# Optimization experiments

Measured on AMD Instinct MI355X. Metric: run time of the kernel, lower is better.

## Reference

```python
import jax, jax.numpy as jnp
import numpy as np

EPS = 1e-5

def _bn(x, g, b, m, v):
    inv = g / jnp.sqrt(v + EPS)
    return x * inv[None, :, None, None] + (b - m * inv)[None, :, None, None]

def _box_conv(x, y_min, y_max, x_min, x_max):
    # Learnable box filter via integral image + bilinear-interpolated corners.
    # x: (N, C, H, W); box params: (C, B). Output: (N, C*B, H, W), area-normalized.
    N, C, H, W = x.shape
    B = y_min.shape[1]
    # padded integral image (N, C, H+1, W+1)
    I = jnp.pad(jnp.cumsum(jnp.cumsum(x, axis=2), axis=3), ((0, 0), (0, 0), (1, 0), (1, 0)))
    iy = jnp.arange(H, dtype=x.dtype)
    ix = jnp.arange(W, dtype=x.dtype)

    def one_box(Ic, ymn, ymx, xmn, xmx):
        # Ic: (N, H+1, W+1); scalar box extents
        y1 = jnp.clip(iy + ymn, 0.0, H)
        y2 = jnp.clip(iy + ymx + 1.0, 0.0, H)
        x1 = jnp.clip(ix + xmn, 0.0, W)
        x2 = jnp.clip(ix + xmx + 1.0, 0.0, W)

        def interp_y(c):  # (H,) -> (N, H, W+1)
            i0 = jnp.clip(jnp.floor(c), 0.0, H - 1).astype(jnp.int32)
            t = (c - i0)[None, :, None]
            return Ic[:, i0, :] * (1.0 - t) + Ic[:, i0 + 1, :] * t

        Gy1, Gy2 = interp_y(y1), interp_y(y2)

        def interp_x(G, c):  # (N, H, W+1), (W,) -> (N, H, W)
            i0 = jnp.clip(jnp.floor(c), 0.0, W - 1).astype(jnp.int32)
            t = (c - i0)[None, None, :]
            return G[:, :, i0] * (1.0 - t) + G[:, :, i0 + 1] * t

        S = interp_x(Gy2, x2) - interp_x(Gy2, x1) - interp_x(Gy1, x2) + interp_x(Gy1, x1)
        area = (ymx - ymn + 1.0) * (xmx - xmn + 1.0)
        return S / area  # (N, H, W)

    f_b = jax.vmap(one_box, in_axes=(None, 0, 0, 0, 0))   # over boxes
    f_cb = jax.vmap(f_b, in_axes=(1, 0, 0, 0, 0))          # over channels
    out = f_cb(I, y_min, y_max, x_min, x_max)              # (C, B, N, H, W)
    return jnp.transpose(out, (2, 0, 1, 3, 4)).reshape(N, C * B, H, W)


def setup_inputs() -> dict:
    key = jax.random.key(0)
    ks = jax.random.split(key, 20)
    N, Cin, H, W = 32, 256, 56, 56
    Cmid, B = 16, 4
    Cbox = Cmid * B
    Cout = 256
    f32 = jnp.float32
    x = jax.random.normal(ks[0], (N, Cin, H, W), f32)
    w1 = jax.random.normal(ks[1], (Cmid, Cin), f32) * 0.05
    g1 = jax.random.uniform(ks[2], (Cmid,), f32, 0.5, 1.5)
    b1 = jax.random.normal(ks[3], (Cmid,), f32) * 0.1
    m1 = jax.random.normal(ks[4], (Cmid,), f32) * 0.1
    v1 = jax.random.uniform(ks[5], (Cmid,), f32, 0.5, 1.5)
    y_min = -jax.random.uniform(ks[6], (Cmid, B), f32) * 10.0
    y_max = jax.random.uniform(ks[7], (Cmid, B), f32) * 10.0
    x_min = -jax.random.uniform(ks[8], (Cmid, B), f32) * 10.0
    x_max = jax.random.uniform(ks[9], (Cmid, B), f32) * 10.0
    g2 = jax.random.uniform(ks[10], (Cbox,), f32, 0.5, 1.5)
    b2 = jax.random.normal(ks[11], (Cbox,), f32) * 0.1
    m2 = jax.random.normal(ks[12], (Cbox,), f32) * 0.1
    v2 = jax.random.uniform(ks[13], (Cbox,), f32, 0.5, 1.5)
    w3 = jax.random.normal(ks[14], (Cout, Cbox), f32) * 0.05
    g3 = jax.random.uniform(ks[15], (Cout,), f32, 0.5, 1.5)
    b3 = jax.random.normal(ks[16], (Cout,), f32) * 0.1
    m3 = jax.random.normal(ks[17], (Cout,), f32) * 0.1
    v3 = jax.random.uniform(ks[18], (Cout,), f32, 0.5, 1.5)
    return {"x": x, "w1": w1, "g1": g1, "b1": b1, "m1": m1, "v1": v1,
            "y_min": y_min, "y_max": y_max, "x_min": x_min, "x_max": x_max,
            "g2": g2, "b2": b2, "m2": m2, "v2": v2,
            "w3": w3, "g3": g3, "b3": b3, "m3": m3, "v3": v3}


def reference(x, w1, g1, b1, m1, v1, y_min, y_max, x_min, x_max,
              g2, b2, m2, v2, w3, g3, b3, m3, v3):
    out = jnp.einsum('nchw,oc->nohw', x, w1)            # 1x1 conv
    out = jax.nn.relu(_bn(out, g1, b1, m1, v1))
    out = _box_conv(out, y_min, y_max, x_min, x_max)    # (N, Cmid*B, H, W)
    out = jax.nn.relu(_bn(out, g2, b2, m2, v2))
    out = jnp.einsum('nchw,oc->nohw', out, w3)          # 1x1 conv
    out = _bn(out, g3, b3, m3, v3)
    return jax.nn.relu(out + x)
```

## Files before the change

kernel.cpp:

```cpp
#include <hip/hip_runtime.h>
#include <hip/hip_bf16.h>
#include <math.h>

#define EPSB 1e-5f

constexpr int NN = 32, CIN = 256, HH = 56, WW = 56, HW = HH * WW;
constexpr int CMID = 16, NB = 4, CBOX = 64, COUT = 256;

typedef __attribute__((ext_vector_type(8))) short short8;
typedef __attribute__((ext_vector_type(4))) float f32x4;

constexpr size_t WS_INV3  = 0;
constexpr size_t WS_B3F   = WS_INV3 + COUT;
constexpr size_t WS_W3B   = WS_B3F + COUT;
constexpr size_t WS_OUT1B = WS_W3B + (size_t)CBOX * COUT / 2;
constexpr size_t WS_OUT2B = WS_OUT1B + (size_t)NN * CMID * HW / 2;

__global__ __launch_bounds__(256) void k1(const float* __restrict__ x,
                                          const float* __restrict__ w1,
                                          const float* __restrict__ g1,
                                          const float* __restrict__ b1,
                                          const float* __restrict__ m1,
                                          const float* __restrict__ v1,
                                          const float* __restrict__ w3,
                                          const float* __restrict__ g3,
                                          const float* __restrict__ b3,
                                          const float* __restrict__ m3,
                                          const float* __restrict__ v3,
                                          float* __restrict__ ws,
                                          __hip_bfloat16* __restrict__ out1b) {
  __shared__ __hip_bfloat16 Xb[64][264];
  __shared__ __hip_bfloat16 Wb[16][264];
  int bid = blockIdx.x;
  int n = bid / 49, hwb = (bid % 49) * 64;
  int tid = threadIdx.x;
  int l = tid & 63, w = tid >> 6;

  if (bid == 0) {
    __hip_bfloat16* w3b = (__hip_bfloat16*)(ws + WS_W3B);
    const float* wp = w3 + tid * 64;
#pragma unroll
    for (int j = 0; j < 64; j += 8) {
      f32x4 a = *reinterpret_cast<const f32x4*>(wp + j);
      f32x4 b = *reinterpret_cast<const f32x4*>(wp + j + 4);
      union { short8 s; __hip_bfloat16 h[8]; } u;
#pragma unroll
      for (int q = 0; q < 4; ++q) { u.h[q] = __float2bfloat16(a[q]); u.h[q + 4] = __float2bfloat16(b[q]); }
      *reinterpret_cast<short8*>(w3b + tid * 64 + j) = u.s;
    }
    float iv = g3[tid] / sqrtf(v3[tid] + EPSB);
    ws[WS_INV3 + tid] = iv;
    ws[WS_B3F + tid] = b3[tid] - m3[tid] * iv;
  }

  {
    int c = tid >> 4, kb = (tid & 15) * 16;
    float inv = g1[c] / sqrtf(v1[c] + EPSB);
    const float* wp = w1 + c * CIN + kb;
#pragma unroll
    for (int j = 0; j < 16; ++j)
      Wb[c][kb + j] = __float2bfloat16(wp[j] * inv);
  }

  {
    const float* xb = x + (size_t)n * CIN * HW + hwb;
    int pxq = (tid & 15) * 4;
    int cio = (tid >> 4) * 2;
#pragma unroll
    for (int p = 0; p < 8; ++p) {
      int ci = p * 32 + cio;
      f32x4 a = *reinterpret_cast<const f32x4*>(xb + (size_t)ci * HW + pxq);
      f32x4 b = *reinterpret_cast<const f32x4*>(xb + (size_t)(ci + 1) * HW + pxq);
#pragma unroll
      for (int j = 0; j < 4; ++j) {
        unsigned lo = (unsigned)__bfloat16_as_ushort(__float2bfloat16(a[j]));
        unsigned hi = (unsigned)__bfloat16_as_ushort(__float2bfloat16(b[j]));
        *reinterpret_cast<unsigned*>(&Xb[pxq + j][ci]) = lo | (hi << 16);
      }
    }
  }
  __syncthreads();

  int pix = 16 * w + (l & 15);
  f32x4 acc = (f32x4)(0.f);
#pragma unroll
  for (int kk = 0; kk < 8; ++kk) {
    int k0 = kk * 32 + (l >> 4) * 8;
    short8 afr = *reinterpret_cast<const short8*>(&Wb[l & 15][k0]);
    short8 bfr = *reinterpret_cast<const short8*>(&Xb[pix][k0]);
    acc = __builtin_amdgcn_mfma_f32_16x16x32_bf16(afr, bfr, acc, 0, 0, 0);
  }

#pragma unroll
  for (int j = 0; j < 4; ++j) {
    int c = (l >> 4) * 4 + j;
    float inv = g1[c] / sqrtf(v1[c] + EPSB);
    float val = acc[j] + (b1[c] - m1[c] * inv);
    out1b[((size_t)n * CMID + c) * HW + hwb + pix] = __float2bfloat16(fmaxf(val, 0.f));
  }
}

__device__ __forceinline__ float bilin(const float* __restrict__ sI, float y, float x) {
  int iy = min((int)y, 55);
  int ix = min((int)x, 55);
  float ty = y - (float)iy;
  float tx = x - (float)ix;
  const float* r = sI + iy * 57 + ix;
  float a = r[0], b = r[1], cc = r[57], d = r[58];
  float g1v = a * (1.f - ty) + cc * ty;
  float g2v = b * (1.f - ty) + d * ty;
  return g1v * (1.f - tx) + g2v * tx;
}

__global__ __launch_bounds__(512) void k2(
    const __hip_bfloat16* __restrict__ out1b,
    const float* __restrict__ y_min, const float* __restrict__ y_max,
    const float* __restrict__ x_min, const float* __restrict__ x_max,
    const float* __restrict__ g2, const float* __restrict__ b2,
    const float* __restrict__ m2, const float* __restrict__ v2,
    __hip_bfloat16* __restrict__ out2b) {
  __shared__ float sI[57 * 57];
  int bid = blockIdx.x;
  int half = bid & 1;
  int c = (bid >> 1) & 15;
  int n = bid >> 5;
  int tid = threadIdx.x;
  int lane = tid & 63, w = tid >> 6;

  if (tid < 57) { sI[tid] = 0.f; sI[tid * 57] = 0.f; }
  const __hip_bfloat16* src = out1b + ((size_t)n * CMID + c) * HW;
  if (tid < HW / 8) {
    int p = tid * 8;
    int h = p / 56, wq = p - h * 56;
    short8 d = ((const short8*)src)[tid];
    const __hip_bfloat16* dp = (const __hip_bfloat16*)&d;
    float* dst = &sI[(h + 1) * 57 + wq + 1];
#pragma unroll
    for (int j = 0; j < 8; ++j) dst[j] = __bfloat162float(dp[j]);
  }
  __syncthreads();

  for (int r = w; r < 56; r += 8) {
    float* row = &sI[(r + 1) * 57 + 1];
    float vv = (lane < 56) ? row[lane] : 0.f;
#pragma unroll
    for (int d = 1; d < 64; d <<= 1) {
      float o = __shfl_up(vv, d, 64);
      if (lane >= d) vv += o;
    }
    if (lane < 56) row[lane] = vv;
  }
  __syncthreads();
  for (int cc = w; cc < 56; cc += 8) {
    float* col = &sI[57 + cc + 1];
    float vv = (lane < 56) ? col[lane * 57] : 0.f;
#pragma unroll
    for (int d = 1; d < 64; d <<= 1) {
      float o = __shfl_up(vv, d, 64);
      if (lane >= d) vv += o;
    }
    if (lane < 56) col[lane * 57] = vv;
  }
  __syncthreads();

  float pymn[NB], pymx[NB], pxmn[NB], pxmx[NB], pinv[NB], pbi[NB], prar[NB];
#pragma unroll
  for (int b = 0; b < NB; ++b) {
    int cb = c * NB + b;
    pymn[b] = y_min[cb]; pymx[b] = y_max[cb];
    pxmn[b] = x_min[cb]; pxmx[b] = x_max[cb];
    float inv = g2[cb] / sqrtf(v2[cb] + EPSB);
    pinv[b] = inv;
    pbi[b] = b2[cb] - m2[cb] * inv;
    prar[b] = 1.f / ((pymx[b] - pymn[b] + 1.f) * (pxmx[b] - pxmn[b] + 1.f));
  }
  __hip_bfloat16* dst0 = out2b + ((size_t)n * CBOX + c * NB) * HW;

  int pend = (half + 1) * (HW / 2);
  for (int p = half * (HW / 2) + tid; p < pend; p += 512) {
    int h = p / 56, wq = p - h * 56;
    float fh = (float)h, fw = (float)wq;
#pragma unroll
    for (int b = 0; b < NB; ++b) {
      float y1 = fminf(fmaxf(fh + pymn[b], 0.f), 56.f);
      float y2 = fminf(fmaxf(fh + pymx[b] + 1.f, 0.f), 56.f);
      float x1 = fminf(fmaxf(fw + pxmn[b], 0.f), 56.f);
      float x2 = fminf(fmaxf(fw + pxmx[b] + 1.f, 0.f), 56.f);
      float S = bilin(sI, y2, x2) - bilin(sI, y2, x1) - bilin(sI, y1, x2) + bilin(sI, y1, x1);
      float val = S * prar[b] * pinv[b] + pbi[b];
      dst0[(size_t)b * HW + p] = __float2bfloat16(fmaxf(val, 0.f));
    }
  }
}

__global__ __launch_bounds__(512) void k3(
    const __hip_bfloat16* __restrict__ out2b,
    const __hip_bfloat16* __restrict__ w3b,
    const float* __restrict__ inv3, const float* __restrict__ b3f,
    const float* __restrict__ x, float* __restrict__ out) {
  __shared__ __hip_bfloat16 T[64][72];
  int bid = blockIdx.x;
  int n = bid / 49, hwb = (bid % 49) * 64;
  int tid = threadIdx.x;
  int l = tid & 63, w = tid >> 6;

  {
    const __hip_bfloat16* srcp = out2b + ((size_t)n * CBOX + l) * HW + hwb + w * 8;
    short8 v = *reinterpret_cast<const short8*>(srcp);
    const __hip_bfloat16* vp = (const __hip_bfloat16*)&v;
#pragma unroll
    for (int i = 0; i < 8; ++i) T[w * 8 + i][l] = vp[i];
  }

  short8 afrag[2][2];
#pragma unroll
  for (int ot = 0; ot < 2; ++ot)
#pragma unroll
    for (int kh = 0; kh < 2; ++kh) {
      int o = w * 32 + ot * 16 + (l & 15);
      int k0 = kh * 32 + (l >> 4) * 8;
      afrag[ot][kh] = *reinterpret_cast<const short8*>(w3b + o * CBOX + k0);
    }

  __syncthreads();

  short8 bfrag[4][2];
#pragma unroll
  for (int pt = 0; pt < 4; ++pt)
#pragma unroll
    for (int kh = 0; kh < 2; ++kh) {
      int pix = pt * 16 + (l & 15);
      int k0 = kh * 32 + (l >> 4) * 8;
      bfrag[pt][kh] = *reinterpret_cast<const short8*>(&T[pix][k0]);
    }

  f32x4 acc[2][4];
#pragma unroll
  for (int ot = 0; ot < 2; ++ot)
#pragma unroll
    for (int pt = 0; pt < 4; ++pt) acc[ot][pt] = (f32x4)(0.f);

#pragma unroll
  for (int ot = 0; ot < 2; ++ot)
#pragma unroll
    for (int pt = 0; pt < 4; ++pt) {
      acc[ot][pt] = __builtin_amdgcn_mfma_f32_16x16x32_bf16(
          afrag[ot][0], bfrag[pt][0], acc[ot][pt], 0, 0, 0);
      acc[ot][pt] = __builtin_amdgcn_mfma_f32_16x16x32_bf16(
          afrag[ot][1], bfrag[pt][1], acc[ot][pt], 0, 0, 0);
    }

  size_t nbase = (size_t)n * COUT * HW + hwb;
#pragma unroll
  for (int ot = 0; ot < 2; ++ot) {
#pragma unroll
    for (int j = 0; j < 4; ++j) {
      int o = w * 32 + ot * 16 + (l >> 4) * 4 + j;
      float iv = inv3[o];
      float bb = b3f[o];
      size_t rowbase = nbase + (size_t)o * HW;
#pragma unroll
      for (int pt = 0; pt < 4; ++pt) {
        int pix = pt * 16 + (l & 15);
        float v = acc[ot][pt][j] * iv + bb + x[rowbase + pix];
        out[rowbase + pix] = fmaxf(v, 0.f);
      }
    }
  }
}

extern "C" void kernel_launch(void* const* d_in, const int* in_sizes, int n_in,
                              void* d_out, int out_size, void* d_ws, size_t ws_size,
                              hipStream_t stream) {
  const float* x   = (const float*)d_in[0];
  const float* w1  = (const float*)d_in[1];
  const float* g1  = (const float*)d_in[2];
  const float* b1  = (const float*)d_in[3];
  const float* m1  = (const float*)d_in[4];
  const float* v1  = (const float*)d_in[5];
  const float* ymn = (const float*)d_in[6];
  const float* ymx = (const float*)d_in[7];
  const float* xmn = (const float*)d_in[8];
  const float* xmx = (const float*)d_in[9];
  const float* g2  = (const float*)d_in[10];
  const float* b2  = (const float*)d_in[11];
  const float* m2  = (const float*)d_in[12];
  const float* v2  = (const float*)d_in[13];
  const float* w3  = (const float*)d_in[14];
  const float* g3  = (const float*)d_in[15];
  const float* b3  = (const float*)d_in[16];
  const float* m3  = (const float*)d_in[17];
  const float* v3  = (const float*)d_in[18];

  float* ws  = (float*)d_ws;
  float* out = (float*)d_out;
  __hip_bfloat16* out1b = (__hip_bfloat16*)(ws + WS_OUT1B);
  __hip_bfloat16* out2b = (__hip_bfloat16*)(ws + WS_OUT2B);
  __hip_bfloat16* w3b   = (__hip_bfloat16*)(ws + WS_W3B);

  k1<<<NN * 49, 256, 0, stream>>>(x, w1, g1, b1, m1, v1,
                                  w3, g3, b3, m3, v3, ws, out1b);
  k2<<<NN * CMID * 2, 512, 0, stream>>>(out1b, ymn, ymx, xmn, xmx,
                                        g2, b2, m2, v2, out2b);
  k3<<<NN * 49, 512, 0, stream>>>(out2b, w3b, ws + WS_INV3, ws + WS_B3F, x, out);
}
```

Measured before the change: 83.66 us.

## Swap MFMA operand order for vectorized epilogue stores and halve box-filter grid

In k1 and k3 the MFMA A/B operands are swapped so each lane's accumulator holds 4 consecutive pixels of one channel. The epilogue can then do 8-byte bf16 stores in k1 and float4 residual loads and output stores in k3, in place of scalar strided accesses. The k1 weight and input staging is widened to 16-byte LDS writes. k2 drops the two-blocks-per-channel split, so each block builds the integral image once and covers all pixels, which removes the duplicated prefix-sum work at the cost of half as many blocks.

```diff
diff --git a/kernel.cpp b/kernel.cpp
--- a/kernel.cpp
+++ b/kernel.cpp
@@ -57,25 +57,32 @@
     int c = tid >> 4, kb = (tid & 15) * 16;
     float inv = g1[c] / sqrtf(v1[c] + EPSB);
     const float* wp = w1 + c * CIN + kb;
-#pragma unroll
-    for (int j = 0; j < 16; ++j)
-      Wb[c][kb + j] = __float2bfloat16(wp[j] * inv);
+    f32x4 a[4];
+#pragma unroll
+    for (int q = 0; q < 4; ++q) a[q] = *reinterpret_cast<const f32x4*>(wp + q * 4);
+    union { short8 s[2]; __hip_bfloat16 h[16]; } u;
+#pragma unroll
+    for (int j = 0; j < 16; ++j) u.h[j] = __float2bfloat16(a[j >> 2][j & 3] * inv);
+    *reinterpret_cast<short8*>(&Wb[c][kb]) = u.s[0];
+    *reinterpret_cast<short8*>(&Wb[c][kb + 8]) = u.s[1];
   }
 
   {
     const float* xb = x + (size_t)n * CIN * HW + hwb;
-    int pxq = (tid & 15) * 4;
-    int cio = (tid >> 4) * 2;
-#pragma unroll
-    for (int p = 0; p < 8; ++p) {
-      int ci = p * 32 + cio;
-      f32x4 a = *reinterpret_cast<const f32x4*>(xb + (size_t)ci * HW + pxq);
-      f32x4 b = *reinterpret_cast<const f32x4*>(xb + (size_t)(ci + 1) * HW + pxq);
-#pragma unroll
-      for (int j = 0; j < 4; ++j) {
-        unsigned lo = (unsigned)__bfloat16_as_ushort(__float2bfloat16(a[j]));
-        unsigned hi = (unsigned)__bfloat16_as_ushort(__float2bfloat16(b[j]));
-        *reinterpret_cast<unsigned*>(&Xb[pxq + j][ci]) = lo | (hi << 16);
+    int px0 = (tid & 15) * 4, ci0 = (tid >> 4) * 16;
+#pragma unroll
+    for (int hh = 0; hh < 2; ++hh) {
+      int cb = ci0 + hh * 8;
+      f32x4 v[8];
+#pragma unroll
+      for (int cj = 0; cj < 8; ++cj)
+        v[cj] = *reinterpret_cast<const f32x4*>(xb + (size_t)(cb + cj) * HW + px0);
+#pragma unroll
+      for (int pj = 0; pj < 4; ++pj) {
+        union { short8 s; __hip_bfloat16 h[8]; } u;
+#pragma unroll
+        for (int cj = 0; cj < 8; ++cj) u.h[cj] = __float2bfloat16(v[cj][pj]);
+        *reinterpret_cast<short8*>(&Xb[px0 + pj][cb]) = u.s;
       }
     }
   }
@@ -86,17 +93,20 @@
 #pragma unroll
   for (int kk = 0; kk < 8; ++kk) {
     int k0 = kk * 32 + (l >> 4) * 8;
-    short8 afr = *reinterpret_cast<const short8*>(&Wb[l & 15][k0]);
-    short8 bfr = *reinterpret_cast<const short8*>(&Xb[pix][k0]);
-    acc = __builtin_amdgcn_mfma_f32_16x16x32_bf16(afr, bfr, acc, 0, 0, 0);
-  }
-
-#pragma unroll
-  for (int j = 0; j < 4; ++j) {
-    int c = (l >> 4) * 4 + j;
+    short8 xfr = *reinterpret_cast<const short8*>(&Xb[pix][k0]);
+    short8 wfr = *reinterpret_cast<const short8*>(&Wb[l & 15][k0]);
+    acc = __builtin_amdgcn_mfma_f32_16x16x32_bf16(xfr, wfr, acc, 0, 0, 0);
+  }
+
+  {
+    int c = l & 15;
+    int px = 16 * w + (l >> 4) * 4;
     float inv = g1[c] / sqrtf(v1[c] + EPSB);
-    float val = acc[j] + (b1[c] - m1[c] * inv);
-    out1b[((size_t)n * CMID + c) * HW + hwb + pix] = __float2bfloat16(fmaxf(val, 0.f));
+    float bb = b1[c] - m1[c] * inv;
+    union { unsigned long long v; __hip_bfloat16 h[4]; } o;
+#pragma unroll
+    for (int j = 0; j < 4; ++j) o.h[j] = __float2bfloat16(fmaxf(acc[j] + bb, 0.f));
+    *reinterpret_cast<unsigned long long*>(out1b + ((size_t)n * CMID + c) * HW + hwb + px) = o.v;
   }
 }
 
@@ -121,9 +131,7 @@
     __hip_bfloat16* __restrict__ out2b) {
   __shared__ float sI[57 * 57];
   int bid = blockIdx.x;
-  int half = bid & 1;
-  int c = (bid >> 1) & 15;
-  int n = bid >> 5;
+  int n = bid >> 4, c = bid & 15;
   int tid = threadIdx.x;
   int lane = tid & 63, w = tid >> 6;
 
@@ -176,8 +184,7 @@
   }
   __hip_bfloat16* dst0 = out2b + ((size_t)n * CBOX + c * NB) * HW;
 
-  int pend = (half + 1) * (HW / 2);
-  for (int p = half * (HW / 2) + tid; p < pend; p += 512) {
+  for (int p = tid; p < HW; p += 512) {
     int h = p / 56, wq = p - h * 56;
     float fh = (float)h, fw = (float)wq;
 #pragma unroll
@@ -212,59 +219,60 @@
     for (int i = 0; i < 8; ++i) T[w * 8 + i][l] = vp[i];
   }
 
-  short8 afrag[2][2];
+  short8 wfrag[2][2];
 #pragma unroll
   for (int ot = 0; ot < 2; ++ot)
 #pragma unroll
     for (int kh = 0; kh < 2; ++kh) {
       int o = w * 32 + ot * 16 + (l & 15);
       int k0 = kh * 32 + (l >> 4) * 8;
-      afrag[ot][kh] = *reinterpret_cast<const short8*>(w3b + o * CBOX + k0);
-    }
-
-  __syncthreads();
-
-  short8 bfrag[4][2];
+      wfrag[ot][kh] = *reinterpret_cast<const short8*>(w3b + o * CBOX + k0);
+    }
+
+  __syncthreads();
+
+  short8 tfrag[4][2];
 #pragma unroll
   for (int pt = 0; pt < 4; ++pt)
 #pragma unroll
     for (int kh = 0; kh < 2; ++kh) {
       int pix = pt * 16 + (l & 15);
       int k0 = kh * 32 + (l >> 4) * 8;
-      bfrag[pt][kh] = *reinterpret_cast<const short8*>(&T[pix][k0]);
-    }
-
-  f32x4 acc[2][4];
-#pragma unroll
-  for (int ot = 0; ot < 2; ++ot)
-#pragma unroll
-    for (int pt = 0; pt < 4; ++pt) acc[ot][pt] = (f32x4)(0.f);
-
-#pragma unroll
-  for (int ot = 0; ot < 2; ++ot)
+      tfrag[pt][kh] = *reinterpret_cast<const short8*>(&T[pix][k0]);
+    }
+
+  f32x4 acc[4][2];
+#pragma unroll
+  for (int pt = 0; pt < 4; ++pt)
+#pragma unroll
+    for (int ot = 0; ot < 2; ++ot) acc[pt][ot] = (f32x4)(0.f);
+
+#pragma unroll
+  for (int pt = 0; pt < 4; ++pt)
+#pragma unroll
+    for (int ot = 0; ot < 2; ++ot) {
+      acc[pt][ot] = __builtin_amdgcn_mfma_f32_16x16x32_bf16(
+          tfrag[pt][0], wfrag[ot][0], acc[pt][ot], 0, 0, 0);
+      acc[pt][ot] = __builtin_amdgcn_mfma_f32_16x16x32_bf16(
+          tfrag[pt][1], wfrag[ot][1], acc[pt][ot], 0, 0, 0);
+    }
+
+  size_t nbase = (size_t)n * COUT * HW + hwb;
+#pragma unroll
+  for (int ot = 0; ot < 2; ++ot) {
+    int o = w * 32 + ot * 16 + (l & 15);
+    float iv = inv3[o];
+    float bb = b3f[o];
+    size_t rowbase = nbase + (size_t)o * HW;
 #pragma unroll
     for (int pt = 0; pt < 4; ++pt) {
-      acc[ot][pt] = __builtin_amdgcn_mfma_f32_16x16x32_bf16(
-          afrag[ot][0], bfrag[pt][0], acc[ot][pt], 0, 0, 0);
-      acc[ot][pt] = __builtin_amdgcn_mfma_f32_16x16x32_bf16(
-          afrag[ot][1], bfrag[pt][1], acc[ot][pt], 0, 0, 0);
-    }
-
-  size_t nbase = (size_t)n * COUT * HW + hwb;
-#pragma unroll
-  for (int ot = 0; ot < 2; ++ot) {
-#pragma unroll
-    for (int j = 0; j < 4; ++j) {
-      int o = w * 32 + ot * 16 + (l >> 4) * 4 + j;
-      float iv = inv3[o];
-      float bb = b3f[o];
-      size_t rowbase = nbase + (size_t)o * HW;
-#pragma unroll
-      for (int pt = 0; pt < 4; ++pt) {
-        int pix = pt * 16 + (l & 15);
-        float v = acc[ot][pt][j] * iv + bb + x[rowbase + pix];
-        out[rowbase + pix] = fmaxf(v, 0.f);
-      }
+      int px0 = pt * 16 + (l >> 4) * 4;
+      f32x4 xv = *reinterpret_cast<const f32x4*>(x + rowbase + px0);
+      f32x4 r;
+#pragma unroll
+      for (int j = 0; j < 4; ++j)
+        r[j] = fmaxf(acc[pt][ot][j] * iv + bb + xv[j], 0.f);
+      *reinterpret_cast<f32x4*>(out + rowbase + px0) = r;
     }
   }
 }
@@ -300,7 +308,7 @@
 
   k1<<<NN * 49, 256, 0, stream>>>(x, w1, g1, b1, m1, v1,
                                   w3, g3, b3, m3, v3, ws, out1b);
-  k2<<<NN * CMID * 2, 512, 0, stream>>>(out1b, ymn, ymx, xmn, xmx,
-                                        g2, b2, m2, v2, out2b);
+  k2<<<NN * CMID, 512, 0, stream>>>(out1b, ymn, ymx, xmn, xmx,
+                                    g2, b2, m2, v2, out2b);
   k3<<<NN * 49, 512, 0, stream>>>(out2b, w3b, ws + WS_INV3, ws + WS_B3F, x, out);
 }
```

Result: no change. 82.45 us (-1.5%).
